# Performance work log

Measured on AMD Instinct MI355X. Metric: run time of the kernel, lower is better.

Reference implementation:

```python
import jax, jax.numpy as jnp
import numpy as np

N_LEVELS = 12
N_FEATURES = 2
LOG2_T = 19
T = 2 ** LOG2_T
BASE_RES = 16
GROWTH = 1.38
RESOLUTIONS = [int(np.floor(BASE_RES * GROWTH ** l)) for l in range(N_LEVELS)]
N_PTS = 1048576

# primes as uint32; XOR/mod-2^19 only depend on low bits, so uint32 wraparound
# multiplication reproduces torch's int64 hash exactly.
P1 = np.uint32(2654435761)
P2 = np.uint32(805459861)

_OFFSETS = jnp.array([[0,0,0],[1,0,0],[0,1,0],[1,1,0],[0,0,1],[1,0,1],[0,1,1],[1,1,1]], dtype=jnp.uint32)  # (8,3)


def setup_inputs() -> dict:
    key = jax.random.key(0)
    k1, k2 = jax.random.split(key)
    x = jax.random.uniform(k1, (N_PTS, 3), dtype=jnp.float32)  # coords in [0,1]
    tables = jax.random.uniform(k2, (N_LEVELS, T, N_FEATURES), dtype=jnp.float32,
                                minval=-1e-4, maxval=1e-4)
    return {"x": x, "tables": tables}


def _encode(x, tables):
    res_arr = jnp.array(RESOLUTIONS, dtype=jnp.float32)  # (L,)

    def level_fn(table, res):
        x_scaled = x * res                      # (N,3)
        x_floor = jnp.floor(x_scaled)
        w = x_scaled - x_floor                  # (N,3) trilinear fractions
        xi = x_floor.astype(jnp.uint32)
        corners = xi[:, None, :] + _OFFSETS[None, :, :]          # (N,8,3)
        h = corners[..., 0] ^ (corners[..., 1] * P1) ^ (corners[..., 2] * P2)
        idx = (h & jnp.uint32(T - 1)).astype(jnp.int32)          # mod 2^19
        feats = table[idx]                                        # (N,8,F) gather
        # weight per corner: prod over dims of (w if offset==1 else 1-w)
        wc = jnp.where(_OFFSETS[None, :, :] == 1, w[:, None, :], 1.0 - w[:, None, :])
        weights = wc.prod(axis=-1)                                # (N,8)
        return (weights[..., None] * feats).sum(axis=1)           # (N,F)

    feats = jax.vmap(level_fn)(tables, res_arr)                   # (L,N,F)
    return feats.transpose(1, 0, 2).reshape(x.shape[0], -1)       # (N, L*F)


def reference(x, tables):
    return _encode(x, tables)
```

## Files before the change

kernel.cpp:

```cpp
#include <hip/hip_runtime.h>


constexpr int NPTS     = 1 << 20;
constexpr int NLEVELS  = 12;
constexpr unsigned T     = 1u << 19;
constexpr unsigned TMASK = T - 1u;
constexpr unsigned P1 = 2654435761u;
constexpr unsigned P2 = 805459861u;

constexpr float WS_SCALE     = 16384.0f;
constexpr float WS_INV_SCALE = 1.0f / 16384.0f;

typedef float    vfloat2 __attribute__((ext_vector_type(2)));
typedef float    vfloat4 __attribute__((ext_vector_type(4)));
typedef _Float16 vhalf2  __attribute__((ext_vector_type(2)));

__constant__ float c_res[NLEVELS] = {16.f, 22.f, 30.f, 42.f, 58.f, 80.f,
                                     110.f, 152.f, 210.f, 290.f, 400.f, 553.f};

__device__ __forceinline__ float2 encode_one_level(
    float px, float py, float pz, float r, const float2* __restrict__ tab)
{
    const float xs = px * r, ys = py * r, zs = pz * r;
    const float xf = floorf(xs), yf = floorf(ys), zf = floorf(zs);
    const float wx = xs - xf, wy = ys - yf, wz = zs - zf;
    const unsigned xi = (unsigned)xf, yi = (unsigned)yf, zi = (unsigned)zf;

    unsigned Y[4];
#pragma unroll
    for (int j = 0; j < 4; ++j) {
        const unsigned oy = j & 1u, oz = (j >> 1) & 1u;
        Y[j] = ((yi + oy) * P1) ^ ((zi + oz) * P2);
    }

    float2 f[8];
    if ((xi & 1u) == 0u) {
#pragma unroll
        for (int j = 0; j < 4; ++j) {
            const unsigned h = (xi ^ Y[j]) & TMASK;
            const vfloat4 q = *reinterpret_cast<const vfloat4*>(
                tab + (h & ~1u));
            const bool hi = (h & 1u) != 0u;
            const float2 e_lo = make_float2(q.x, q.y);
            const float2 e_hi = make_float2(q.z, q.w);
            f[2 * j + 0] = hi ? e_hi : e_lo;
            f[2 * j + 1] = hi ? e_lo : e_hi;
        }
    } else {
#pragma unroll
        for (int j = 0; j < 4; ++j) {
            const unsigned h0 = (xi ^ Y[j]) & TMASK;
            const unsigned h1 = ((xi + 1u) ^ Y[j]) & TMASK;
            f[2 * j + 0] = tab[h0];
            f[2 * j + 1] = tab[h1];
        }
    }

    float f0 = 0.f, f1 = 0.f;
#pragma unroll
    for (int c = 0; c < 8; ++c) {
        const unsigned ox = c & 1u, oy = (c >> 1) & 1u, oz = (c >> 2) & 1u;
        const float w = (ox ? wx : 1.f - wx) *
                        (oy ? wy : 1.f - wy) *
                        (oz ? wz : 1.f - wz);
        f0 += w * f[c].x;
        f1 += w * f[c].y;
    }
    return make_float2(f0, f1);
}

__global__ __launch_bounds__(256, 8)
void hashgrid_level_kernel(const float* __restrict__ x,
                           const float* __restrict__ tables,
                           _Float16* __restrict__ ws)
{
    const int n = blockIdx.x * 256 + threadIdx.x;
    const int l = blockIdx.y;

    const float px = x[3 * n + 0];
    const float py = x[3 * n + 1];
    const float pz = x[3 * n + 2];

    const float2* __restrict__ tab =
        reinterpret_cast<const float2*>(tables) + (size_t)l * T;

    const float2 f = encode_one_level(px, py, pz, c_res[l], tab);
    vhalf2 h = {(_Float16)(f.x * WS_SCALE), (_Float16)(f.y * WS_SCALE)};
    __builtin_nontemporal_store(
        h, reinterpret_cast<vhalf2*>(ws) + ((size_t)l * NPTS + n));
}

__global__ __launch_bounds__(256)
void hashgrid_transpose_kernel(const _Float16* __restrict__ ws,
                               float* __restrict__ out)
{
    __shared__ float lds[512 * 25];
    const int t = threadIdx.x;
    const int base = blockIdx.x * 512;

#pragma unroll
    for (int l = 0; l < NLEVELS; ++l) {
#pragma unroll
        for (int k = 0; k < 2; ++k) {
            const int p = t + 256 * k;
            const vhalf2 h = __builtin_nontemporal_load(
                reinterpret_cast<const vhalf2*>(ws) + ((size_t)l * NPTS + base + p));
            lds[p * 25 + 2 * l + 0] = (float)h.x * WS_INV_SCALE;
            lds[p * 25 + 2 * l + 1] = (float)h.y * WS_INV_SCALE;
        }
    }
    __syncthreads();

    float* __restrict__ ob = out + (size_t)base * 24;
#pragma unroll
    for (int i = 0; i < 12; ++i) {
        const int j  = i * 256 + t;
        const int f0 = 4 * j;
        const int p  = f0 / 24;
        const int c  = f0 % 24;
        vfloat4 v = {lds[p * 25 + c + 0], lds[p * 25 + c + 1],
                     lds[p * 25 + c + 2], lds[p * 25 + c + 3]};
        __builtin_nontemporal_store(v, reinterpret_cast<vfloat4*>(ob + f0));
    }
}

__global__ __launch_bounds__(256, 4)
void hashgrid_fused_kernel(const float* __restrict__ x,
                           const float* __restrict__ tables,
                           float* __restrict__ out)
{
    const int n = blockIdx.x * 256 + threadIdx.x;
    const float px = x[3 * n + 0];
    const float py = x[3 * n + 1];
    const float pz = x[3 * n + 2];

    float o[2 * NLEVELS];
#pragma unroll
    for (int l = 0; l < NLEVELS; ++l) {
        const float2* __restrict__ tab =
            reinterpret_cast<const float2*>(tables) + (size_t)l * T;
        const float2 f = encode_one_level(px, py, pz, c_res[l], tab);
        o[2 * l + 0] = f.x;
        o[2 * l + 1] = f.y;
    }
    float4* __restrict__ op = reinterpret_cast<float4*>(out + (size_t)n * 24);
#pragma unroll
    for (int i = 0; i < 6; ++i)
        op[i] = make_float4(o[4*i+0], o[4*i+1], o[4*i+2], o[4*i+3]);
}

extern "C" void kernel_launch(void* const* d_in, const int* in_sizes, int n_in,
                              void* d_out, int out_size, void* d_ws, size_t ws_size,
                              hipStream_t stream)
{
    const float* x      = reinterpret_cast<const float*>(d_in[0]);
    const float* tables = reinterpret_cast<const float*>(d_in[1]);
    float* out          = reinterpret_cast<float*>(d_out);

    const size_t ws_needed = (size_t)NLEVELS * NPTS * 2 * sizeof(_Float16);
    if (ws_size >= ws_needed) {
        _Float16* ws = reinterpret_cast<_Float16*>(d_ws);
        dim3 grid(NPTS / 256, NLEVELS);
        hashgrid_level_kernel<<<grid, 256, 0, stream>>>(x, tables, ws);
        hashgrid_transpose_kernel<<<NPTS / 512, 256, 0, stream>>>(ws, out);
    } else {
        hashgrid_fused_kernel<<<NPTS / 256, 256, 0, stream>>>(x, tables, out);
    }
}
```

Measured before the change: 381.3 us.

## Replace level-split plus transpose with cooperative kernel syncing grid per level

Replaces the two-kernel scheme (a per-level kernel writing fp16 to workspace, then a transpose kernel) with a single persistent kernel. Each thread handles four points across all levels, and a grid-wide barrier after each level keeps every block on the same hash table, so that level's table stays hot in cache. Results are held in registers as scaled fp16 and written directly in the final layout, which removes the workspace round trip. The costs are eleven grid syncs, higher register pressure from the 4x12 accumulators, and reliance on cooperative-launch support, with a fallback that uses only block-level syncs.

Result: slower. 1.302 ms (+241.4%).

```diff
diff --git a/kernel.cpp b/kernel.cpp
--- a/kernel.cpp
+++ b/kernel.cpp
@@ -1,4 +1,7 @@
 #include <hip/hip_runtime.h>
+#include <hip/hip_cooperative_groups.h>
+
+namespace cg = cooperative_groups;
 
 
 constexpr int NPTS     = 1 << 20;
@@ -15,8 +18,8 @@
 typedef float    vfloat4 __attribute__((ext_vector_type(4)));
 typedef _Float16 vhalf2  __attribute__((ext_vector_type(2)));
 
-__constant__ float c_res[NLEVELS] = {16.f, 22.f, 30.f, 42.f, 58.f, 80.f,
-                                     110.f, 152.f, 210.f, 290.f, 400.f, 553.f};
+constexpr float k_res[NLEVELS] = {16.f, 22.f, 30.f, 42.f, 58.f, 80.f,
+                                  110.f, 152.f, 210.f, 290.f, 400.f, 553.f};
 
 __device__ __forceinline__ float2 encode_one_level(
     float px, float py, float pz, float r, const float2* __restrict__ tab)
@@ -69,84 +72,56 @@
     return make_float2(f0, f1);
 }
 
-__global__ __launch_bounds__(256, 8)
-void hashgrid_level_kernel(const float* __restrict__ x,
-                           const float* __restrict__ tables,
-                           _Float16* __restrict__ ws)
+template <bool SYNC>
+__global__ __launch_bounds__(256, 4)
+void hashgrid_coop_kernel(const float* __restrict__ x,
+                          const float* __restrict__ tables,
+                          float* __restrict__ out)
 {
-    const int n = blockIdx.x * 256 + threadIdx.x;
-    const int l = blockIdx.y;
+    const int tid = blockIdx.x * 256 + threadIdx.x;
+    const int n0  = tid * 4;
 
-    const float px = x[3 * n + 0];
-    const float py = x[3 * n + 1];
-    const float pz = x[3 * n + 2];
+    const vfloat4* __restrict__ xv =
+        reinterpret_cast<const vfloat4*>(x) + (size_t)tid * 3;
+    const vfloat4 a = xv[0], b = xv[1], c = xv[2];
+    const float px[4] = {a.x, a.w, b.z, c.y};
+    const float py[4] = {a.y, b.x, b.w, c.z};
+    const float pz[4] = {a.z, b.y, c.x, c.w};
 
-    const float2* __restrict__ tab =
-        reinterpret_cast<const float2*>(tables) + (size_t)l * T;
+    vhalf2 acc[4][NLEVELS];
 
-    const float2 f = encode_one_level(px, py, pz, c_res[l], tab);
-    vhalf2 h = {(_Float16)(f.x * WS_SCALE), (_Float16)(f.y * WS_SCALE)};
-    __builtin_nontemporal_store(
-        h, reinterpret_cast<vhalf2*>(ws) + ((size_t)l * NPTS + n));
-}
-
-__global__ __launch_bounds__(256)
-void hashgrid_transpose_kernel(const _Float16* __restrict__ ws,
-                               float* __restrict__ out)
-{
-    __shared__ float lds[512 * 25];
-    const int t = threadIdx.x;
-    const int base = blockIdx.x * 512;
-
-#pragma unroll
-    for (int l = 0; l < NLEVELS; ++l) {
-#pragma unroll
-        for (int k = 0; k < 2; ++k) {
-            const int p = t + 256 * k;
-            const vhalf2 h = __builtin_nontemporal_load(
-                reinterpret_cast<const vhalf2*>(ws) + ((size_t)l * NPTS + base + p));
-            lds[p * 25 + 2 * l + 0] = (float)h.x * WS_INV_SCALE;
-            lds[p * 25 + 2 * l + 1] = (float)h.y * WS_INV_SCALE;
-        }
-    }
-    __syncthreads();
-
-    float* __restrict__ ob = out + (size_t)base * 24;
-#pragma unroll
-    for (int i = 0; i < 12; ++i) {
-        const int j  = i * 256 + t;
-        const int f0 = 4 * j;
-        const int p  = f0 / 24;
-        const int c  = f0 % 24;
-        vfloat4 v = {lds[p * 25 + c + 0], lds[p * 25 + c + 1],
-                     lds[p * 25 + c + 2], lds[p * 25 + c + 3]};
-        __builtin_nontemporal_store(v, reinterpret_cast<vfloat4*>(ob + f0));
-    }
-}
-
-__global__ __launch_bounds__(256, 4)
-void hashgrid_fused_kernel(const float* __restrict__ x,
-                           const float* __restrict__ tables,
-                           float* __restrict__ out)
-{
-    const int n = blockIdx.x * 256 + threadIdx.x;
-    const float px = x[3 * n + 0];
-    const float py = x[3 * n + 1];
-    const float pz = x[3 * n + 2];
-
-    float o[2 * NLEVELS];
 #pragma unroll
     for (int l = 0; l < NLEVELS; ++l) {
         const float2* __restrict__ tab =
             reinterpret_cast<const float2*>(tables) + (size_t)l * T;
-        const float2 f = encode_one_level(px, py, pz, c_res[l], tab);
-        o[2 * l + 0] = f.x;
-        o[2 * l + 1] = f.y;
+        const float r = k_res[l];
+#pragma unroll
+        for (int k = 0; k < 4; ++k) {
+            const float2 f = encode_one_level(px[k], py[k], pz[k], r, tab);
+            acc[k][l] = vhalf2{(_Float16)(f.x * WS_SCALE),
+                               (_Float16)(f.y * WS_SCALE)};
+        }
+        if (l < NLEVELS - 1) {
+            if constexpr (SYNC) {
+                cg::this_grid().sync();
+            } else {
+                __syncthreads();
+            }
+        }
     }
-    float4* __restrict__ op = reinterpret_cast<float4*>(out + (size_t)n * 24);
+
 #pragma unroll
-    for (int i = 0; i < 6; ++i)
-        op[i] = make_float4(o[4*i+0], o[4*i+1], o[4*i+2], o[4*i+3]);
+    for (int k = 0; k < 4; ++k) {
+        float* __restrict__ op = out + (size_t)(n0 + k) * 24;
+#pragma unroll
+        for (int i = 0; i < 6; ++i) {
+            const vfloat4 v = {(float)acc[k][2 * i + 0].x * WS_INV_SCALE,
+                               (float)acc[k][2 * i + 0].y * WS_INV_SCALE,
+                               (float)acc[k][2 * i + 1].x * WS_INV_SCALE,
+                               (float)acc[k][2 * i + 1].y * WS_INV_SCALE};
+            __builtin_nontemporal_store(v, reinterpret_cast<vfloat4*>(op) + i);
+        }
+    }
 }
 
 extern "C" void kernel_launch(void* const* d_in, const int* in_sizes, int n_in,
@@ -157,13 +132,31 @@
     const float* tables = reinterpret_cast<const float*>(d_in[1]);
     float* out          = reinterpret_cast<float*>(d_out);
 
-    const size_t ws_needed = (size_t)NLEVELS * NPTS * 2 * sizeof(_Float16);
-    if (ws_size >= ws_needed) {
-        _Float16* ws = reinterpret_cast<_Float16*>(d_ws);
-        dim3 grid(NPTS / 256, NLEVELS);
-        hashgrid_level_kernel<<<grid, 256, 0, stream>>>(x, tables, ws);
-        hashgrid_transpose_kernel<<<NPTS / 512, 256, 0, stream>>>(ws, out);
-    } else {
-        hashgrid_fused_kernel<<<NPTS / 256, 256, 0, stream>>>(x, tables, out);
+    constexpr int GRID = NPTS / (256 * 4);
+
+    static int mode = -1;
+    if (mode < 0) {
+        int dev = 0;
+        (void)hipGetDevice(&dev);
+        hipDeviceProp_t prop{};
+        (void)hipGetDeviceProperties(&prop, dev);
+        int nb = 0;
+        (void)hipOccupancyMaxActiveBlocksPerMultiprocessor(
+            &nb, hashgrid_coop_kernel<true>, 256, 0);
+        const int cus = prop.multiProcessorCount > 0 ? prop.multiProcessorCount : 256;
+        const int needed_per_cu = (GRID + cus - 1) / cus;
+        mode = (prop.cooperativeLaunch != 0 && nb >= needed_per_cu) ? 1 : 0;
     }
+
+    if (mode == 1) {
+        void* args[] = {(void*)&x, (void*)&tables, (void*)&out};
+        const hipError_t e = hipLaunchCooperativeKernel(
+            reinterpret_cast<void*>(hashgrid_coop_kernel<true>),
+            dim3(GRID), dim3(256), args, 0, stream);
+        if (e == hipSuccess) return;
+        mode = 0;
+    }
+
+    hashgrid_coop_kernel<false><<<dim3(GRID), dim3(256), 0, stream>>>(
+        x, tables, out);
 }
```

## Spatially bucket-sort points before per-level hash gathers

Applied to the files above, without the earlier changes.

Adds a counting sort of points into a 32^3 spatial grid (histogram, scan, scatter). The per-level gather then runs over the sorted points, so neighbouring threads touch nearby hash-table entries and the cache hit rate should rise. A finish kernel scatters results back to the original order. This adds four extra passes with atomics, a single-block scan, and uncoalesced 96-byte output writes, in exchange for better locality in the table gathers.

Result: slower. 689.8 us (+80.9%).

```diff
diff --git a/kernel.cpp b/kernel.cpp
--- a/kernel.cpp
+++ b/kernel.cpp
@@ -7,6 +7,8 @@
 constexpr unsigned TMASK = T - 1u;
 constexpr unsigned P1 = 2654435761u;
 constexpr unsigned P2 = 805459861u;
+
+constexpr int NBUCK = 32 * 32 * 32;
 
 constexpr float WS_SCALE     = 16384.0f;
 constexpr float WS_INV_SCALE = 1.0f / 16384.0f;
@@ -69,6 +71,120 @@
     return make_float2(f0, f1);
 }
 
+
+__global__ __launch_bounds__(256)
+void key_hist_kernel(const float* __restrict__ x,
+                     unsigned* __restrict__ key,
+                     unsigned* __restrict__ hist)
+{
+    const int n = blockIdx.x * 256 + threadIdx.x;
+    const float px = x[3 * n + 0];
+    const float py = x[3 * n + 1];
+    const float pz = x[3 * n + 2];
+    const unsigned bx = min((unsigned)(px * 32.0f), 31u);
+    const unsigned by = min((unsigned)(py * 32.0f), 31u);
+    const unsigned bz = min((unsigned)(pz * 32.0f), 31u);
+    const unsigned k = (bx << 10) | (by << 5) | bz;
+    key[n] = k;
+    atomicAdd(&hist[k], 1u);
+}
+
+__global__ __launch_bounds__(1024)
+void scan_kernel(const unsigned* __restrict__ hist,
+                 unsigned* __restrict__ cursor)
+{
+    __shared__ unsigned sblk[1024];
+    const int t = threadIdx.x;
+    const int base = t * 32;
+
+    unsigned v[32];
+    unsigned sum = 0;
+#pragma unroll
+    for (int i = 0; i < 32; ++i) {
+        v[i] = hist[base + i];
+        sum += v[i];
+    }
+    sblk[t] = sum;
+    __syncthreads();
+
+    for (int off = 1; off < 1024; off <<= 1) {
+        const unsigned add = (t >= off) ? sblk[t - off] : 0u;
+        __syncthreads();
+        sblk[t] += add;
+        __syncthreads();
+    }
+    unsigned acc = sblk[t] - sum;
+#pragma unroll
+    for (int i = 0; i < 32; ++i) {
+        cursor[base + i] = acc;
+        acc += v[i];
+    }
+}
+
+__global__ __launch_bounds__(256)
+void scatter_kernel(const float* __restrict__ x,
+                    const unsigned* __restrict__ key,
+                    unsigned* __restrict__ cursor,
+                    float* __restrict__ xs,
+                    unsigned* __restrict__ s2o)
+{
+    const int n = blockIdx.x * 256 + threadIdx.x;
+    const unsigned k = key[n];
+    const unsigned s = atomicAdd(&cursor[k], 1u);
+    xs[3 * s + 0] = x[3 * n + 0];
+    xs[3 * s + 1] = x[3 * n + 1];
+    xs[3 * s + 2] = x[3 * n + 2];
+    s2o[s] = n;
+}
+
+__global__ __launch_bounds__(256, 8)
+void gather_kernel(const float* __restrict__ xs,
+                   const float* __restrict__ tables,
+                   _Float16* __restrict__ ws)
+{
+    const int s = blockIdx.x * 256 + threadIdx.x;
+    const int l = blockIdx.y;
+
+    const float px = xs[3 * s + 0];
+    const float py = xs[3 * s + 1];
+    const float pz = xs[3 * s + 2];
+
+    const float2* __restrict__ tab =
+        reinterpret_cast<const float2*>(tables) + (size_t)l * T;
+
+    const float2 f = encode_one_level(px, py, pz, c_res[l], tab);
+    vhalf2 h = {(_Float16)(f.x * WS_SCALE), (_Float16)(f.y * WS_SCALE)};
+    __builtin_nontemporal_store(
+        h, reinterpret_cast<vhalf2*>(ws) + ((size_t)l * NPTS + s));
+}
+
+__global__ __launch_bounds__(256)
+void finish_kernel(const _Float16* __restrict__ ws,
+                   const unsigned* __restrict__ s2o,
+                   float* __restrict__ out)
+{
+    const int s = blockIdx.x * 256 + threadIdx.x;
+    const unsigned o = s2o[s];
+
+    float vals[2 * NLEVELS];
+#pragma unroll
+    for (int l = 0; l < NLEVELS; ++l) {
+        const vhalf2 h = __builtin_nontemporal_load(
+            reinterpret_cast<const vhalf2*>(ws) + ((size_t)l * NPTS + s));
+        vals[2 * l + 0] = (float)h.x * WS_INV_SCALE;
+        vals[2 * l + 1] = (float)h.y * WS_INV_SCALE;
+    }
+
+    float* __restrict__ op = out + (size_t)o * 24;
+#pragma unroll
+    for (int i = 0; i < 6; ++i) {
+        const vfloat4 v = {vals[4 * i + 0], vals[4 * i + 1],
+                           vals[4 * i + 2], vals[4 * i + 3]};
+        __builtin_nontemporal_store(v, reinterpret_cast<vfloat4*>(op) + i);
+    }
+}
+
+
 __global__ __launch_bounds__(256, 8)
 void hashgrid_level_kernel(const float* __restrict__ x,
                            const float* __restrict__ tables,
@@ -149,6 +265,7 @@
         op[i] = make_float4(o[4*i+0], o[4*i+1], o[4*i+2], o[4*i+3]);
 }
 
+
 extern "C" void kernel_launch(void* const* d_in, const int* in_sizes, int n_in,
                               void* d_out, int out_size, void* d_ws, size_t ws_size,
                               hipStream_t stream)
@@ -157,13 +274,39 @@
     const float* tables = reinterpret_cast<const float*>(d_in[1]);
     float* out          = reinterpret_cast<float*>(d_out);
 
-    const size_t ws_needed = (size_t)NLEVELS * NPTS * 2 * sizeof(_Float16);
-    if (ws_size >= ws_needed) {
+    const size_t SZ_WS16 = (size_t)NLEVELS * NPTS * 2 * sizeof(_Float16);
+    const size_t SZ_XS   = (size_t)NPTS * 3 * sizeof(float);
+    const size_t SZ_S2O  = (size_t)NPTS * sizeof(unsigned);
+    const size_t SZ_KEY  = (size_t)NPTS * sizeof(unsigned);
+    const size_t SZ_H    = (size_t)NBUCK * sizeof(unsigned);
+    const size_t need_sorted = SZ_WS16 + SZ_XS + SZ_S2O + SZ_KEY + 2 * SZ_H;
+
+    if (ws_size >= need_sorted) {
+        char* p = reinterpret_cast<char*>(d_ws);
+        _Float16* ws16   = reinterpret_cast<_Float16*>(p);  p += SZ_WS16;
+        float*    xs     = reinterpret_cast<float*>(p);     p += SZ_XS;
+        unsigned* s2o    = reinterpret_cast<unsigned*>(p);  p += SZ_S2O;
+        unsigned* key    = reinterpret_cast<unsigned*>(p);  p += SZ_KEY;
+        unsigned* hist   = reinterpret_cast<unsigned*>(p);  p += SZ_H;
+        unsigned* cursor = reinterpret_cast<unsigned*>(p);
+
+        hipMemsetAsync(hist, 0, SZ_H, stream);
+        key_hist_kernel<<<NPTS / 256, 256, 0, stream>>>(x, key, hist);
+        scan_kernel<<<1, 1024, 0, stream>>>(hist, cursor);
+        scatter_kernel<<<NPTS / 256, 256, 0, stream>>>(x, key, cursor, xs, s2o);
+        gather_kernel<<<dim3(NPTS / 256, NLEVELS), 256, 0, stream>>>(
+            xs, tables, ws16);
+        finish_kernel<<<NPTS / 256, 256, 0, stream>>>(ws16, s2o, out);
+        return;
+    }
+
+    if (ws_size >= SZ_WS16) {
         _Float16* ws = reinterpret_cast<_Float16*>(d_ws);
         dim3 grid(NPTS / 256, NLEVELS);
         hashgrid_level_kernel<<<grid, 256, 0, stream>>>(x, tables, ws);
         hashgrid_transpose_kernel<<<NPTS / 512, 256, 0, stream>>>(ws, out);
-    } else {
-        hashgrid_fused_kernel<<<NPTS / 256, 256, 0, stream>>>(x, tables, out);
-    }
-}
+        return;
+    }
+
+    hashgrid_fused_kernel<<<NPTS / 256, 256, 0, stream>>>(x, tables, out);
+}
```
